# Performance work log

Hardware: AMD Instinct MI355X
Metric: run time of the kernel (lower is better)

## Reference

```python
import jax, jax.numpy as jnp
import numpy as np

NUM_ATOMS = 4_000_000
NUM_TYPES = 11

def setup_inputs() -> dict:
    key = jax.random.key(0)
    k1, k2 = jax.random.split(key)
    input_coords = jax.random.normal(k1, (3 * NUM_ATOMS,), dtype=jnp.float32)
    atom_types = jax.random.randint(k2, (NUM_ATOMS,), 0, NUM_TYPES, dtype=jnp.int64)
    return {"input_coords": input_coords, "atom_types": atom_types, "num_atom_types": NUM_TYPES}

def reference(input_coords, atom_types, num_atom_types):
    # counts per atom type  [T]
    counts = jnp.bincount(atom_types, length=num_atom_types).astype(jnp.int32)
    # exclusive prefix sum -> bucket offsets  [T]
    offsets = (jnp.cumsum(counts) - counts).astype(jnp.int32)
    # stable sort by type reproduces the C++ bucket fill order:
    # atoms of the same type keep their original relative order.
    perm = jnp.argsort(atom_types, stable=True)  # [N] source index for each output slot
    coords3 = input_coords.reshape(-1, 3)        # [N,3]
    typed_coords = coords3[perm].reshape(-1)     # [3N] type-grouped flat coords
    return typed_coords, counts, offsets
```

## Files before the change

kernel.cpp:

```cpp
#include <hip/hip_runtime.h>

#define NTYPES 11
#define BLOCK  256
#define ITEMS  8
#define CHUNK  (BLOCK * ITEMS)
#define PERMAX 32
#define SCATTER_GRID 1536

__global__ __launch_bounds__(BLOCK) void hist_kernel(
    const int* __restrict__ types, int N, int B, int* __restrict__ bc) {
  __shared__ int shCnt[NTYPES];
  const int tid = threadIdx.x;
  const int b = blockIdx.x;
  if (tid < NTYPES) shCnt[tid] = 0;
  __syncthreads();

  const int run = b * CHUNK + tid * ITEMS;
  int cnt[NTYPES];
#pragma unroll
  for (int t = 0; t < NTYPES; ++t) cnt[t] = 0;

  if (run < N) {
    const int4* p = (const int4*)(types + run);
    int4 a0 = p[0], a1 = p[1];
    int ty[ITEMS] = {a0.x, a0.y, a0.z, a0.w, a1.x, a1.y, a1.z, a1.w};
#pragma unroll
    for (int k = 0; k < ITEMS; ++k) {
#pragma unroll
      for (int t = 0; t < NTYPES; ++t) cnt[t] += (ty[k] == t) ? 1 : 0;
    }
  }

  const int lane = tid & 63;
#pragma unroll
  for (int t = 0; t < NTYPES; ++t) {
    int v = cnt[t];
    for (int o = 32; o >= 1; o >>= 1) v += __shfl_down(v, o);
    if (lane == 0) atomicAdd(&shCnt[t], v);
  }
  __syncthreads();
  if (tid < NTYPES) bc[tid * B + b] = shCnt[tid];
}

__global__ __launch_bounds__(NTYPES * 64) void scan_kernel(
    const int* __restrict__ bc, int B, int* __restrict__ scanOut,
    int* __restrict__ offs, float* __restrict__ outTail) {
  __shared__ int totals[NTYPES];
  const int lane = threadIdx.x & 63;
  const int t = threadIdx.x >> 6;
  const int per = (B + 63) >> 6;
  const int base = lane * per;

  int x[PERMAX];
#pragma unroll
  for (int j = 0; j < PERMAX; ++j) {
    const int idx = base + j;
    x[j] = (j < per && idx < B) ? bc[t * B + idx] : 0;
  }
  int s = 0;
#pragma unroll
  for (int j = 0; j < PERMAX; ++j) s += x[j];

  int incl = s;
#pragma unroll
  for (int o = 1; o < 64; o <<= 1) {
    int v = __shfl_up(incl, o);
    if (lane >= o) incl += v;
  }
  int run = incl - s;
  const int total = __shfl(incl, 63);

#pragma unroll
  for (int j = 0; j < PERMAX; ++j) {
    const int idx = base + j;
    if (j < per && idx < B) scanOut[t * B + idx] = run;
    run += x[j];
  }
  if (lane == 0) totals[t] = total;
  __syncthreads();

  if (threadIdx.x == 0) {
    int off = 0;
    for (int u = 0; u < NTYPES; ++u) {
      const int c = totals[u];
      offs[u] = off;
      outTail[u] = (float)c;
      outTail[NTYPES + u] = (float)off;
      off += c;
    }
  }
}

__global__ __launch_bounds__(BLOCK) void scatter_kernel(
    const float* __restrict__ coords, const int* __restrict__ types,
    const int* __restrict__ scanOut, const int* __restrict__ offs, int N,
    int B, float* __restrict__ out) {
  __shared__ float shC[CHUNK * 3];
  __shared__ int wtot[NTYPES][4];
  __shared__ int shOff[NTYPES + 1];
  __shared__ int shDelta[NTYPES];

  const int tid = threadIdx.x;
  const int lane = tid & 63;
  const int wave = tid >> 6;

  for (int b = blockIdx.x; b < B; b += gridDim.x) {
    __syncthreads();

    const int run = b * CHUNK + tid * ITEMS;
    const bool active = (run < N);

    int ty[ITEMS];
    int cnt[NTYPES];
#pragma unroll
    for (int t = 0; t < NTYPES; ++t) cnt[t] = 0;
#pragma unroll
    for (int k = 0; k < ITEMS; ++k) ty[k] = -1;

    float c[ITEMS * 3];
    if (active) {
      const int4* p = (const int4*)(types + run);
      int4 a0 = p[0], a1 = p[1];
      int tt[ITEMS] = {a0.x, a0.y, a0.z, a0.w, a1.x, a1.y, a1.z, a1.w};
#pragma unroll
      for (int k = 0; k < ITEMS; ++k) ty[k] = tt[k];
      const float4* cp = (const float4*)(coords + (size_t)run * 3);
#pragma unroll
      for (int q = 0; q < (ITEMS * 3) / 4; ++q) {
        float4 v = cp[q];
        c[4 * q + 0] = v.x;
        c[4 * q + 1] = v.y;
        c[4 * q + 2] = v.z;
        c[4 * q + 3] = v.w;
      }
#pragma unroll
      for (int k = 0; k < ITEMS; ++k) {
#pragma unroll
        for (int t = 0; t < NTYPES; ++t) cnt[t] += (ty[k] == t) ? 1 : 0;
      }
    }

    int pk[6];
#pragma unroll
    for (int q = 0; q < 5; ++q) pk[q] = cnt[2 * q] | (cnt[2 * q + 1] << 16);
    pk[5] = cnt[10];
#pragma unroll
    for (int o = 1; o < 64; o <<= 1) {
      int v0 = __shfl_up(pk[0], o);
      int v1 = __shfl_up(pk[1], o);
      int v2 = __shfl_up(pk[2], o);
      int v3 = __shfl_up(pk[3], o);
      int v4 = __shfl_up(pk[4], o);
      int v5 = __shfl_up(pk[5], o);
      if (lane >= o) {
        pk[0] += v0;
        pk[1] += v1;
        pk[2] += v2;
        pk[3] += v3;
        pk[4] += v4;
        pk[5] += v5;
      }
    }
    int rank[NTYPES];
#pragma unroll
    for (int t = 0; t < NTYPES; ++t) {
      const int incl = (pk[t >> 1] >> ((t & 1) * 16)) & 0xFFFF;
      if (lane == 63) wtot[t][wave] = incl;
      rank[t] = incl - cnt[t];
    }
    __syncthreads();

    if (tid < NTYPES) {
      int loc = 0;
      for (int u = 0; u < tid; ++u)
        loc += wtot[u][0] + wtot[u][1] + wtot[u][2] + wtot[u][3];
      shOff[tid] = loc;
      shDelta[tid] = 3 * (offs[tid] + scanOut[tid * B + b] - loc);
      if (tid == NTYPES - 1) {
        shOff[NTYPES] =
            loc + wtot[tid][0] + wtot[tid][1] + wtot[tid][2] + wtot[tid][3];
      }
    }
    __syncthreads();

#pragma unroll
    for (int t = 0; t < NTYPES; ++t) {
      int wb = 0;
#pragma unroll
      for (int w = 0; w < 3; ++w) wb += (w < wave) ? wtot[t][w] : 0;
      rank[t] += wb + shOff[t];
    }

    if (active) {
#pragma unroll
      for (int k = 0; k < ITEMS; ++k) {
        const int t0 = ty[k];
        int slot = 0;
#pragma unroll
        for (int t = 0; t < NTYPES; ++t) {
          if (t0 == t) {
            slot = rank[t];
            rank[t] += 1;
          }
        }
        shC[3 * slot + 0] = c[3 * k + 0];
        shC[3 * slot + 1] = c[3 * k + 1];
        shC[3 * slot + 2] = c[3 * k + 2];
      }
    }
    __syncthreads();

    const int total = shOff[NTYPES];
    int offr[NTYPES];
    int dlt[NTYPES];
#pragma unroll
    for (int t = 0; t < NTYPES; ++t) {
      offr[t] = shOff[t];
      dlt[t] = shDelta[t];
    }
#pragma unroll
    for (int k = 0; k < ITEMS; ++k) {
      const int s = k * BLOCK + tid;
      if (s < total) {
        int d = dlt[0];
#pragma unroll
        for (int t = 1; t < NTYPES; ++t) d = (s >= offr[t]) ? dlt[t] : d;
        const int src = 3 * s;
        out[src + d + 0] = shC[src + 0];
        out[src + d + 1] = shC[src + 1];
        out[src + d + 2] = shC[src + 2];
      }
    }
  }
}

extern "C" void kernel_launch(void* const* d_in, const int* in_sizes, int n_in,
                              void* d_out, int out_size, void* d_ws,
                              size_t ws_size, hipStream_t stream) {
  const float* coords = (const float*)d_in[0];
  const int* types = (const int*)d_in[1];
  const int N = in_sizes[1];
  const int B = (N + CHUNK - 1) / CHUNK;

  int* bc = (int*)d_ws;
  int* scanOut = bc + NTYPES * B;
  int* offs = scanOut + NTYPES * B;
  float* out = (float*)d_out;
  float* outTail = out + (size_t)3 * N;

  const int G = (B < SCATTER_GRID) ? B : SCATTER_GRID;

  hist_kernel<<<B, BLOCK, 0, stream>>>(types, N, B, bc);
  scan_kernel<<<1, NTYPES * 64, 0, stream>>>(bc, B, scanOut, offs, outTail);
  scatter_kernel<<<G, BLOCK, 0, stream>>>(coords, types, scanOut, offs, N, B,
                                          out);
}
```

Before: 142.3 us.

## Scatter coords directly to global memory, dropping shared-memory staging and grid-stride loop

The scatter kernel no longer stages coordinates in a 24KB shared-memory buffer to coalesce the global writes. Each thread now writes its 8 atoms' xyz straight to their final output slots, and the grid-stride loop is replaced by one block per chunk. This removes two barriers, the LDS traffic and the LDS occupancy limit. In exchange the global stores become scattered 12-byte writes across 11 type buckets instead of contiguous runs.

Result: slower. 148.1 us (+4.1%).

```diff
diff --git a/kernel.cpp b/kernel.cpp
--- a/kernel.cpp
+++ b/kernel.cpp
@@ -5,7 +5,6 @@
 #define ITEMS  8
 #define CHUNK  (BLOCK * ITEMS)
 #define PERMAX 32
-#define SCATTER_GRID 1536
 
 __global__ __launch_bounds__(BLOCK) void hist_kernel(
     const int* __restrict__ types, int N, int B, int* __restrict__ bc) {
@@ -95,141 +94,101 @@
     const float* __restrict__ coords, const int* __restrict__ types,
     const int* __restrict__ scanOut, const int* __restrict__ offs, int N,
     int B, float* __restrict__ out) {
-  __shared__ float shC[CHUNK * 3];
   __shared__ int wtot[NTYPES][4];
-  __shared__ int shOff[NTYPES + 1];
-  __shared__ int shDelta[NTYPES];
+  __shared__ int shBase[NTYPES];
 
   const int tid = threadIdx.x;
+  const int b = blockIdx.x;
   const int lane = tid & 63;
   const int wave = tid >> 6;
-
-  for (int b = blockIdx.x; b < B; b += gridDim.x) {
-    __syncthreads();
-
-    const int run = b * CHUNK + tid * ITEMS;
-    const bool active = (run < N);
-
-    int ty[ITEMS];
-    int cnt[NTYPES];
-#pragma unroll
-    for (int t = 0; t < NTYPES; ++t) cnt[t] = 0;
-#pragma unroll
-    for (int k = 0; k < ITEMS; ++k) ty[k] = -1;
-
-    float c[ITEMS * 3];
-    if (active) {
-      const int4* p = (const int4*)(types + run);
-      int4 a0 = p[0], a1 = p[1];
-      int tt[ITEMS] = {a0.x, a0.y, a0.z, a0.w, a1.x, a1.y, a1.z, a1.w};
-#pragma unroll
-      for (int k = 0; k < ITEMS; ++k) ty[k] = tt[k];
-      const float4* cp = (const float4*)(coords + (size_t)run * 3);
-#pragma unroll
-      for (int q = 0; q < (ITEMS * 3) / 4; ++q) {
-        float4 v = cp[q];
-        c[4 * q + 0] = v.x;
-        c[4 * q + 1] = v.y;
-        c[4 * q + 2] = v.z;
-        c[4 * q + 3] = v.w;
+  const int run = b * CHUNK + tid * ITEMS;
+  const bool active = (run < N);
+
+  int ty[ITEMS];
+  int cnt[NTYPES];
+#pragma unroll
+  for (int t = 0; t < NTYPES; ++t) cnt[t] = 0;
+#pragma unroll
+  for (int k = 0; k < ITEMS; ++k) ty[k] = -1;
+
+  float c[ITEMS * 3];
+  if (active) {
+    const int4* p = (const int4*)(types + run);
+    int4 a0 = p[0], a1 = p[1];
+    int tt[ITEMS] = {a0.x, a0.y, a0.z, a0.w, a1.x, a1.y, a1.z, a1.w};
+#pragma unroll
+    for (int k = 0; k < ITEMS; ++k) ty[k] = tt[k];
+    const float4* cp = (const float4*)(coords + (size_t)run * 3);
+#pragma unroll
+    for (int q = 0; q < (ITEMS * 3) / 4; ++q) {
+      float4 v = cp[q];
+      c[4 * q + 0] = v.x;
+      c[4 * q + 1] = v.y;
+      c[4 * q + 2] = v.z;
+      c[4 * q + 3] = v.w;
+    }
+#pragma unroll
+    for (int k = 0; k < ITEMS; ++k) {
+#pragma unroll
+      for (int t = 0; t < NTYPES; ++t) cnt[t] += (ty[k] == t) ? 1 : 0;
+    }
+  }
+
+  int pk[6];
+#pragma unroll
+  for (int q = 0; q < 5; ++q) pk[q] = cnt[2 * q] | (cnt[2 * q + 1] << 16);
+  pk[5] = cnt[10];
+#pragma unroll
+  for (int o = 1; o < 64; o <<= 1) {
+    int v0 = __shfl_up(pk[0], o);
+    int v1 = __shfl_up(pk[1], o);
+    int v2 = __shfl_up(pk[2], o);
+    int v3 = __shfl_up(pk[3], o);
+    int v4 = __shfl_up(pk[4], o);
+    int v5 = __shfl_up(pk[5], o);
+    if (lane >= o) {
+      pk[0] += v0;
+      pk[1] += v1;
+      pk[2] += v2;
+      pk[3] += v3;
+      pk[4] += v4;
+      pk[5] += v5;
+    }
+  }
+  int rank[NTYPES];
+#pragma unroll
+  for (int t = 0; t < NTYPES; ++t) {
+    const int incl = (pk[t >> 1] >> ((t & 1) * 16)) & 0xFFFF;
+    if (lane == 63) wtot[t][wave] = incl;
+    rank[t] = incl - cnt[t];
+  }
+  if (tid < NTYPES) shBase[tid] = offs[tid] + scanOut[tid * B + b];
+  __syncthreads();
+
+#pragma unroll
+  for (int t = 0; t < NTYPES; ++t) {
+    int wb = 0;
+#pragma unroll
+    for (int w = 0; w < 3; ++w) wb += (w < wave) ? wtot[t][w] : 0;
+    rank[t] += wb + shBase[t];
+  }
+
+  if (active) {
+#pragma unroll
+    for (int k = 0; k < ITEMS; ++k) {
+      const int t0 = ty[k];
+      int slot = 0;
+#pragma unroll
+      for (int t = 0; t < NTYPES; ++t) {
+        if (t0 == t) {
+          slot = rank[t];
+          rank[t] += 1;
+        }
       }
-#pragma unroll
-      for (int k = 0; k < ITEMS; ++k) {
-#pragma unroll
-        for (int t = 0; t < NTYPES; ++t) cnt[t] += (ty[k] == t) ? 1 : 0;
-      }
-    }
-
-    int pk[6];
-#pragma unroll
-    for (int q = 0; q < 5; ++q) pk[q] = cnt[2 * q] | (cnt[2 * q + 1] << 16);
-    pk[5] = cnt[10];
-#pragma unroll
-    for (int o = 1; o < 64; o <<= 1) {
-      int v0 = __shfl_up(pk[0], o);
-      int v1 = __shfl_up(pk[1], o);
-      int v2 = __shfl_up(pk[2], o);
-      int v3 = __shfl_up(pk[3], o);
-      int v4 = __shfl_up(pk[4], o);
-      int v5 = __shfl_up(pk[5], o);
-      if (lane >= o) {
-        pk[0] += v0;
-        pk[1] += v1;
-        pk[2] += v2;
-        pk[3] += v3;
-        pk[4] += v4;
-        pk[5] += v5;
-      }
-    }
-    int rank[NTYPES];
-#pragma unroll
-    for (int t = 0; t < NTYPES; ++t) {
-      const int incl = (pk[t >> 1] >> ((t & 1) * 16)) & 0xFFFF;
-      if (lane == 63) wtot[t][wave] = incl;
-      rank[t] = incl - cnt[t];
-    }
-    __syncthreads();
-
-    if (tid < NTYPES) {
-      int loc = 0;
-      for (int u = 0; u < tid; ++u)
-        loc += wtot[u][0] + wtot[u][1] + wtot[u][2] + wtot[u][3];
-      shOff[tid] = loc;
-      shDelta[tid] = 3 * (offs[tid] + scanOut[tid * B + b] - loc);
-      if (tid == NTYPES - 1) {
-        shOff[NTYPES] =
-            loc + wtot[tid][0] + wtot[tid][1] + wtot[tid][2] + wtot[tid][3];
-      }
-    }
-    __syncthreads();
-
-#pragma unroll
-    for (int t = 0; t < NTYPES; ++t) {
-      int wb = 0;
-#pragma unroll
-      for (int w = 0; w < 3; ++w) wb += (w < wave) ? wtot[t][w] : 0;
-      rank[t] += wb + shOff[t];
-    }
-
-    if (active) {
-#pragma unroll
-      for (int k = 0; k < ITEMS; ++k) {
-        const int t0 = ty[k];
-        int slot = 0;
-#pragma unroll
-        for (int t = 0; t < NTYPES; ++t) {
-          if (t0 == t) {
-            slot = rank[t];
-            rank[t] += 1;
-          }
-        }
-        shC[3 * slot + 0] = c[3 * k + 0];
-        shC[3 * slot + 1] = c[3 * k + 1];
-        shC[3 * slot + 2] = c[3 * k + 2];
-      }
-    }
-    __syncthreads();
-
-    const int total = shOff[NTYPES];
-    int offr[NTYPES];
-    int dlt[NTYPES];
-#pragma unroll
-    for (int t = 0; t < NTYPES; ++t) {
-      offr[t] = shOff[t];
-      dlt[t] = shDelta[t];
-    }
-#pragma unroll
-    for (int k = 0; k < ITEMS; ++k) {
-      const int s = k * BLOCK + tid;
-      if (s < total) {
-        int d = dlt[0];
-#pragma unroll
-        for (int t = 1; t < NTYPES; ++t) d = (s >= offr[t]) ? dlt[t] : d;
-        const int src = 3 * s;
-        out[src + d + 0] = shC[src + 0];
-        out[src + d + 1] = shC[src + 1];
-        out[src + d + 2] = shC[src + 2];
-      }
+      const int dst = 3 * slot;
+      out[dst + 0] = c[3 * k + 0];
+      out[dst + 1] = c[3 * k + 1];
+      out[dst + 2] = c[3 * k + 2];
     }
   }
 }
@@ -248,10 +207,8 @@
   float* out = (float*)d_out;
   float* outTail = out + (size_t)3 * N;
 
-  const int G = (B < SCATTER_GRID) ? B : SCATTER_GRID;
-
   hist_kernel<<<B, BLOCK, 0, stream>>>(types, N, B, bc);
   scan_kernel<<<1, NTYPES * 64, 0, stream>>>(bc, B, scanOut, offs, outTail);
-  scatter_kernel<<<G, BLOCK, 0, stream>>>(coords, types, scanOut, offs, N, B,
+  scatter_kernel<<<B, BLOCK, 0, stream>>>(coords, types, scanOut, offs, N, B,
                                           out);
 }
```
